# Kernel tuning notes

Hardware: AMD Instinct MI355X
Metric: run time of the kernel (lower is better)

Reference implementation:

```python
import jax, jax.numpy as jnp
import numpy as np

N_NODES = 65536
N_EDGES = 524288
N_GRAPHS = 512
G_NODES = 10000
NUM_DISEASES = 2000
IN_DIM = 128
HID = 256  # 2 * IN_DIM (z_emb concat feat)
D_FEAT = 512
C_FEAT = 512
MAX_Z = 4000


def setup_inputs() -> dict:
    key = jax.random.key(0)
    ks = jax.random.split(key, 20)
    rn = lambda k, shape: jax.random.normal(k, shape, dtype=jnp.float32) * 0.05
    return {
        "z": jax.random.randint(ks[0], (N_NODES,), 0, MAX_Z),
        "node_id": jnp.sort(jax.random.randint(ks[1], (N_NODES,), 0, G_NODES)),
        "src": jax.random.randint(ks[2], (N_EDGES,), 0, N_NODES),
        "dst": jax.random.randint(ks[3], (N_EDGES,), 0, N_NODES),
        "graph_ids": jnp.sort(jax.random.randint(ks[4], (N_NODES,), 0, N_GRAPHS)),
        "z_table": rn(ks[5], (MAX_Z, IN_DIM)),
        "d_feat_tab": rn(ks[6], (G_NODES, D_FEAT)),
        "c_feat_tab": rn(ks[7], (G_NODES, C_FEAT)),
        "Wd": rn(ks[8], (D_FEAT, IN_DIM)),
        "Wc": rn(ks[9], (C_FEAT, IN_DIM)),
        "gin_W1": rn(ks[10], (HID, HID)), "gin_b1": jnp.zeros((HID,), jnp.float32),
        "gin_W2": rn(ks[11], (HID, HID)), "gin_b2": jnp.zeros((HID,), jnp.float32),
        "sage_Wself": rn(ks[12], (HID, HID)),
        "sage_Wneigh": rn(ks[13], (HID, HID)),
        "sage_b": jnp.zeros((HID,), jnp.float32),
        "lin1_W": rn(ks[14], (HID, HID)), "lin1_b": jnp.zeros((HID,), jnp.float32),
        "lin2_W": rn(ks[15], (HID, 1)), "lin2_b": jnp.zeros((1,), jnp.float32),
    }


def reference(z, node_id, src, dst, graph_ids, z_table, d_feat_tab, c_feat_tab,
              Wd, Wc, gin_W1, gin_b1, gin_W2, gin_b2,
              sage_Wself, sage_Wneigh, sage_b, lin1_W, lin1_b, lin2_W, lin2_b):
    # --- input feature construction (Model.forward) ---
    z_emb = z_table[z]                               # [N, IN_DIM]
    d_proj = d_feat_tab[node_id] @ Wd                # d_fc (bias=False)
    c_proj = c_feat_tab[node_id] @ Wc                # c_fc (bias=False)
    disease = (node_id <= NUM_DISEASES)[:, None]
    # node_id is sorted -> masked concat order == node order
    feat = jnp.where(disease, d_proj, c_proj)        # [N, IN_DIM]
    x = jnp.concatenate([z_emb, feat], axis=1)       # [N, HID]
    # --- GINConv: sum aggregation, eps=0, mlp = Lin->ReLU->Lin ---
    agg = jax.ops.segment_sum(x[src], dst, num_segments=N_NODES)
    h = x + agg
    h = jax.nn.relu(h @ gin_W1 + gin_b1) @ gin_W2 + gin_b2
    # --- SAGEConv('mean'): fc_self(h) + fc_neigh(mean_neighbors) + bias ---
    deg = jax.ops.segment_sum(jnp.ones((N_EDGES,), h.dtype), dst, num_segments=N_NODES)
    mean_n = jax.ops.segment_sum(h[src], dst, num_segments=N_NODES) / jnp.maximum(deg, 1.0)[:, None]
    h = h @ sage_Wself + mean_n @ sage_Wneigh + sage_b
    # --- per-graph max pooling readout ---
    g = jax.ops.segment_max(h, graph_ids, num_segments=N_GRAPHS, indices_are_sorted=True)
    g = jnp.where(jnp.isfinite(g), g, 0.0)           # guard empty graphs
    # --- head: Linear -> ReLU -> (dropout p=0, eval) -> Linear ---
    h = jax.nn.relu(g @ lin1_W + lin1_b)
    return h @ lin2_W + lin2_b                       # [N_GRAPHS, 1]
```

## Files before the change

kernel.cpp:

```cpp
#include <hip/hip_runtime.h>
#include <hip/hip_bf16.h>

#define N_NODES     65536
#define N_EDGES     524288
#define N_GRAPHS    512
#define G_NODES_N   10000
#define NUM_DIS     2000
#define IN_DIM      128
#define HID         256
#define D_FEAT      512
#define MAX_Z       4000
#define POOL_SPLIT  8

typedef _Float16 half8 __attribute__((ext_vector_type(8)));
typedef float    f32x4 __attribute__((ext_vector_type(4)));

typedef __attribute__((address_space(1))) const void as1_void;
typedef __attribute__((address_space(3))) void       as3_void;

__global__ __launch_bounds__(256) void prep_kernel(
    const float* __restrict__ Ws, const float* __restrict__ Wn,
    const float* __restrict__ Wd, const float* __restrict__ Wc,
    const float* __restrict__ W1, const float* __restrict__ W2,
    const float* __restrict__ z_table,
    const int* __restrict__ z, const int* __restrict__ node_id,
    _Float16* __restrict__ WsT, _Float16* __restrict__ WnT,
    _Float16* __restrict__ WdT, _Float16* __restrict__ WcT,
    _Float16* __restrict__ W12P, _Float16* __restrict__ zt16,
    int2* __restrict__ zn2, int* __restrict__ cnt, int* __restrict__ flags)
{
    const int b = blockIdx.x;
    const int tid = threadIdx.x;
    if (b < 64) {
        __shared__ float tile[64][65];
        const float* W; _Float16* T; int K, N, k0, n0;
        if (b < 32) {
            const int mat = b >> 4, t = b & 15;
            K = HID; N = HID; k0 = (t >> 2) * 64; n0 = (t & 3) * 64;
            W = (mat == 0) ? Ws : Wn;
            T = (mat == 0) ? WsT : WnT;
        } else {
            const int bb = b - 32;
            const int mat = bb >> 4, t = bb & 15;
            K = D_FEAT; N = IN_DIM; k0 = (t >> 1) * 64; n0 = (t & 1) * 64;
            W = (mat == 0) ? Wd : Wc;
            T = (mat == 0) ? WdT : WcT;
        }
        const int tx = tid & 63, ty = tid >> 6;
        #pragma unroll
        for (int r = 0; r < 64; r += 4)
            tile[r + ty][tx] = W[(size_t)(k0 + r + ty) * N + n0 + tx];
        __syncthreads();
        #pragma unroll
        for (int c = 0; c < 64; c += 4)
            T[(size_t)(n0 + c + ty) * K + k0 + tx] = (_Float16)tile[tx][c + ty];
    } else if (b < 576) {
        const int bb = b - 64;
        const int mat = bb >> 8;
        const int k = bb & 255;
        const int n = tid;
        const float* W = mat ? W2 : W1;
        const float v = W[(size_t)k * HID + n];
        const size_t idx = (size_t)(mat * 8 + (k >> 5)) * 8192
                         + (size_t)((((k >> 3) & 3) * 256 + n) * 8 + (k & 7));
        W12P[idx] = (_Float16)v;
    } else if (b < 826) {
        const size_t base = ((size_t)(b - 576) * 256 + tid) * 8;
        const float4 f0 = *(const float4*)(z_table + base);
        const float4 f1 = *(const float4*)(z_table + base + 4);
        half8 h;
        h[0]=(_Float16)f0.x; h[1]=(_Float16)f0.y; h[2]=(_Float16)f0.z; h[3]=(_Float16)f0.w;
        h[4]=(_Float16)f1.x; h[5]=(_Float16)f1.y; h[6]=(_Float16)f1.z; h[7]=(_Float16)f1.w;
        *(half8*)(zt16 + base) = h;
    } else if (b < 890) {
        const int base = (b - 826) * 1024 + tid * 4;
        *(int4*)(cnt + base) = make_int4(0, 0, 0, 0);
        if (b == 826 && tid < 128) flags[tid] = 0;
    } else {
        const int i = (b - 890) * 256 + tid;
        zn2[i] = make_int2(z[i], node_id[i]);
    }
}

__global__ __launch_bounds__(256) void proj_mfma_kernel(
    const float* __restrict__ dtab, const float* __restrict__ ctab,
    const _Float16* __restrict__ WdT, const _Float16* __restrict__ WcT,
    _Float16* __restrict__ proj)
{
    __shared__ _Float16 Alds[128 * 40];
    __shared__ _Float16 Blds[128 * 40];
    const int blk = blockIdx.x;
    const float* tab; const _Float16* WT; int base, M, bm;
    if (blk < 16) { tab = dtab; WT = WdT; base = 0;           M = NUM_DIS + 1;             bm = blk * 128; }
    else          { tab = ctab; WT = WcT; base = NUM_DIS + 1; M = G_NODES_N - NUM_DIS - 1; bm = (blk - 16) * 128; }
    const int tid  = threadIdx.x;
    const int wave = tid >> 6, lane = tid & 63;
    const int q    = lane >> 4, l16 = lane & 15;
    const int mbase = (wave & 1) * 64, nbase = (wave >> 1) * 64;
    const int r = tid >> 1, s = tid & 1;

    f32x4 acc[4][4] = {};

    for (int kc = 0; kc < 16; ++kc) {
        const int k0 = kc * 32;
        const int arow = min(bm + r, M - 1);
        const float* gA = tab + (size_t)(base + arow) * D_FEAT + k0 + s * 16;
        const _Float16* gB = WT + (size_t)r * D_FEAT + k0 + s * 16;
        const float4 f0 = ((const float4*)gA)[0];
        const float4 f1 = ((const float4*)gA)[1];
        const float4 f2 = ((const float4*)gA)[2];
        const float4 f3 = ((const float4*)gA)[3];
        const half8 hb0 = *(const half8*)gB;
        const half8 hb1 = *(const half8*)(gB + 8);
        half8 h0, h1;
        h0[0]=(_Float16)f0.x; h0[1]=(_Float16)f0.y; h0[2]=(_Float16)f0.z; h0[3]=(_Float16)f0.w;
        h0[4]=(_Float16)f1.x; h0[5]=(_Float16)f1.y; h0[6]=(_Float16)f1.z; h0[7]=(_Float16)f1.w;
        h1[0]=(_Float16)f2.x; h1[1]=(_Float16)f2.y; h1[2]=(_Float16)f2.z; h1[3]=(_Float16)f2.w;
        h1[4]=(_Float16)f3.x; h1[5]=(_Float16)f3.y; h1[6]=(_Float16)f3.z; h1[7]=(_Float16)f3.w;
        __syncthreads();
        *(half8*)&Alds[r * 40 + s * 16]     = h0;
        *(half8*)&Alds[r * 40 + s * 16 + 8] = h1;
        *(half8*)&Blds[r * 40 + s * 16]     = hb0;
        *(half8*)&Blds[r * 40 + s * 16 + 8] = hb1;
        __syncthreads();
        half8 a[4], b[4];
        #pragma unroll
        for (int i = 0; i < 4; ++i)
            a[i] = *(const half8*)&Alds[(mbase + i * 16 + l16) * 40 + q * 8];
        #pragma unroll
        for (int j = 0; j < 4; ++j)
            b[j] = *(const half8*)&Blds[(nbase + j * 16 + l16) * 40 + q * 8];
        #pragma unroll
        for (int i = 0; i < 4; ++i)
            #pragma unroll
            for (int j = 0; j < 4; ++j)
                acc[i][j] = __builtin_amdgcn_mfma_f32_16x16x32_f16(a[i], b[j], acc[i][j], 0, 0, 0);
    }

    #pragma unroll
    for (int j = 0; j < 4; ++j) {
        const int colg = nbase + j * 16 + l16;
        #pragma unroll
        for (int i = 0; i < 4; ++i) {
            #pragma unroll
            for (int rr = 0; rr < 4; ++rr) {
                const int row = bm + mbase + i * 16 + q * 4 + rr;
                if (row < M)
                    proj[(size_t)(base + row) * IN_DIM + colg] = (_Float16)acc[i][j][rr];
            }
        }
    }
}

__global__ __launch_bounds__(256) void hist_kernel(
    const int* __restrict__ dst, int* __restrict__ cnt)
{
    const int e = blockIdx.x * 256 + threadIdx.x;
    if (e < N_EDGES) atomicAdd(&cnt[dst[e]], 1);
}

__global__ __launch_bounds__(256) void scan_fused_kernel(
    const int* __restrict__ cnt, int* __restrict__ row_ptr,
    int* __restrict__ fill, int* __restrict__ flags)
{
    __shared__ int a[256], b[256];
    __shared__ int sums[64];
    __shared__ int segbase;
    const int t = threadIdx.x;
    const int blk = blockIdx.x;
    const int base = blk * 1024 + t * 4;
    const int4 c = *(const int4*)(cnt + base);
    const int s = c.x + c.y + c.z + c.w;
    a[t] = s;
    __syncthreads();
    int* in = a; int* out = b;
    for (int off = 1; off < 256; off <<= 1) {
        out[t] = in[t] + ((t >= off) ? in[t - off] : 0);
        __syncthreads();
        int* tmp = in; in = out; out = tmp;
    }
    if (t == 0) {
        atomicExch(&flags[64 + blk], in[255]);
        __threadfence();
        atomicAdd(&flags[0], 1);
        while (atomicAdd(&flags[0], 0) < 64) {}
    }
    __syncthreads();
    if (t < 64) sums[t] = atomicAdd(&flags[64 + t], 0);
    __syncthreads();
    if (t == 0) {
        int pfx = 0;
        for (int i = 0; i < blk; ++i) pfx += sums[i];
        segbase = pfx;
        if (blk == 63) {
            int tot = pfx;
            for (int i = blk; i < 64; ++i) tot += sums[i];
            row_ptr[N_NODES] = tot;
        }
    }
    __syncthreads();
    const int run = in[t] - s + segbase;
    int4 r;
    r.x = run; r.y = run + c.x; r.z = r.y + c.y; r.w = r.z + c.z;
    *(int4*)(row_ptr + base) = r;
    *(int4*)(fill + base) = r;
}

__global__ __launch_bounds__(256) void scatter_kernel(
    const int* __restrict__ src, const int* __restrict__ dst,
    const int2* __restrict__ zn2,
    int* __restrict__ fill, int* __restrict__ col, int2* __restrict__ colzn)
{
    const int e = blockIdx.x * 256 + threadIdx.x;
    if (e < N_EDGES) {
        const int s = src[e];
        const int pos = atomicAdd(&fill[dst[e]], 1);
        col[pos] = s;
        colzn[pos] = zn2[s];
    }
}

__global__ __launch_bounds__(256) void gin_fused_kernel(
    const int* __restrict__ row_ptr, const int2* __restrict__ colzn,
    const int2* __restrict__ zn2,
    const _Float16* __restrict__ zt16, const _Float16* __restrict__ proj,
    const _Float16* __restrict__ W12P,
    const float* __restrict__ b1, const float* __restrict__ b2,
    _Float16* __restrict__ H)
{
    __shared__ _Float16 Apanel[32 * 264];
    __shared__ _Float16 Blds[2][8192];

    const int bm   = blockIdx.x * 32;
    const int tid  = threadIdx.x;
    const int wave = tid >> 6, lane = tid & 63;
    const int q    = lane >> 4, l16 = lane & 15;
    const int nbase = wave * 64;

    auto stage = [&](int c, int buf) {
        const _Float16* src = W12P + (size_t)c * 8192;
        #pragma unroll
        for (int tt = 0; tt < 4; ++tt) {
            const int seg = (wave * 4 + tt) * 64 + lane;
            __builtin_amdgcn_global_load_lds((as1_void*)(src + seg * 8),
                (as3_void*)&Blds[buf][(wave * 4 + tt) * 64 * 8], 16, 0, 0);
        }
    };

    stage(0, 0);

    {
        const int r = tid >> 3, p = tid & 7;
        const int gr = bm + r;
        const int beg = row_ptr[gr], end = row_ptr[gr + 1];
        float za[16], pa[16];
        {
            const int2 zn = zn2[gr];
            const half8* zp = (const half8*)(zt16 + (size_t)zn.x * IN_DIM + p * 16);
            const half8* pp = (const half8*)(proj + (size_t)zn.y * IN_DIM + p * 16);
            const half8 z0 = zp[0], z1 = zp[1], p0 = pp[0], p1 = pp[1];
            #pragma unroll
            for (int i = 0; i < 8; ++i) {
                za[i] = (float)z0[i]; za[8 + i] = (float)z1[i];
                pa[i] = (float)p0[i]; pa[8 + i] = (float)p1[i];
            }
        }
        int e = beg;
        for (; e + 2 <= end; e += 2) {
            const int2 znA = colzn[e];
            const int2 znB = colzn[e + 1];
            const half8* zpA = (const half8*)(zt16 + (size_t)znA.x * IN_DIM + p * 16);
            const half8* ppA = (const half8*)(proj + (size_t)znA.y * IN_DIM + p * 16);
            const half8* zpB = (const half8*)(zt16 + (size_t)znB.x * IN_DIM + p * 16);
            const half8* ppB = (const half8*)(proj + (size_t)znB.y * IN_DIM + p * 16);
            const half8 zA0 = zpA[0], zA1 = zpA[1], pA0 = ppA[0], pA1 = ppA[1];
            const half8 zB0 = zpB[0], zB1 = zpB[1], pB0 = ppB[0], pB1 = ppB[1];
            #pragma unroll
            for (int i = 0; i < 8; ++i) {
                za[i]     += (float)zA0[i] + (float)zB0[i];
                za[8 + i] += (float)zA1[i] + (float)zB1[i];
                pa[i]     += (float)pA0[i] + (float)pB0[i];
                pa[8 + i] += (float)pA1[i] + (float)pB1[i];
            }
        }
        if (e < end) {
            const int2 zn = colzn[e];
            const half8* zp = (const half8*)(zt16 + (size_t)zn.x * IN_DIM + p * 16);
            const half8* pp = (const half8*)(proj + (size_t)zn.y * IN_DIM + p * 16);
            const half8 z0 = zp[0], z1 = zp[1], p0 = pp[0], p1 = pp[1];
            #pragma unroll
            for (int i = 0; i < 8; ++i) {
                za[i] += (float)z0[i]; za[8 + i] += (float)z1[i];
                pa[i] += (float)p0[i]; pa[8 + i] += (float)p1[i];
            }
        }
        half8 oz0, oz1, op0, op1;
        #pragma unroll
        for (int i = 0; i < 8; ++i) {
            oz0[i] = (_Float16)za[i];     oz1[i] = (_Float16)za[8 + i];
            op0[i] = (_Float16)pa[i];     op1[i] = (_Float16)pa[8 + i];
        }
        *(half8*)&Apanel[r * 264 + p * 16]           = oz0;
        *(half8*)&Apanel[r * 264 + p * 16 + 8]       = oz1;
        *(half8*)&Apanel[r * 264 + 128 + p * 16]     = op0;
        *(half8*)&Apanel[r * 264 + 128 + p * 16 + 8] = op1;
    }
    __syncthreads();

    f32x4 acc[2][4] = {};
    int pb = 0;
    for (int c = 0; c < 16; ++c) {
        if (c + 1 < 16) stage(c + 1, pb ^ 1);
        if (c == 8) {
            #pragma unroll
            for (int j = 0; j < 4; ++j) {
                const int colg = nbase + j * 16 + l16;
                const float bv = b1[colg];
                #pragma unroll
                for (int i = 0; i < 2; ++i)
                    #pragma unroll
                    for (int rr = 0; rr < 4; ++rr) {
                        const float v = fmaxf(acc[i][j][rr] + bv, 0.0f);
                        Apanel[(i * 16 + q * 4 + rr) * 264 + colg] = (_Float16)v;
                        acc[i][j][rr] = 0.0f;
                    }
            }
            __syncthreads();
        }
        const int kl = (c & 7) * 32;
        half8 a[2], b[4];
        #pragma unroll
        for (int i = 0; i < 2; ++i)
            a[i] = *(const half8*)&Apanel[(i * 16 + l16) * 264 + kl + q * 8];
        #pragma unroll
        for (int j = 0; j < 4; ++j)
            b[j] = *(const half8*)&Blds[pb][(q * 256 + nbase + j * 16 + l16) * 8];
        #pragma unroll
        for (int i = 0; i < 2; ++i)
            #pragma unroll
            for (int j = 0; j < 4; ++j)
                acc[i][j] = __builtin_amdgcn_mfma_f32_16x16x32_f16(a[i], b[j], acc[i][j], 0, 0, 0);
        __syncthreads();
        pb ^= 1;
    }

    #pragma unroll
    for (int j = 0; j < 4; ++j) {
        const int colg = nbase + j * 16 + l16;
        const float bv = b2[colg];
        #pragma unroll
        for (int i = 0; i < 2; ++i)
            #pragma unroll
            for (int rr = 0; rr < 4; ++rr) {
                const int rowg = bm + i * 16 + q * 4 + rr;
                H[(size_t)rowg * HID + colg] = (_Float16)(acc[i][j][rr] + bv);
            }
    }
}

__global__ __launch_bounds__(256) void csr_agg_kernel(
    const int* __restrict__ row_ptr, const int* __restrict__ col,
    const _Float16* __restrict__ F, _Float16* __restrict__ OUT)
{
    const int t = blockIdx.x * 256 + threadIdx.x;
    const int d = t >> 5;
    const int q = t & 31;
    const int beg = row_ptr[d];
    const int end = row_ptr[d + 1];
    float acc[8] = {0.f,0.f,0.f,0.f,0.f,0.f,0.f,0.f};
    int e = beg;
    for (; e + 4 <= end; e += 4) {
        const int s0 = col[e],     s1 = col[e + 1];
        const int s2 = col[e + 2], s3 = col[e + 3];
        const half8 v0 = *(const half8*)(F + (size_t)s0 * HID + q * 8);
        const half8 v1 = *(const half8*)(F + (size_t)s1 * HID + q * 8);
        const half8 v2 = *(const half8*)(F + (size_t)s2 * HID + q * 8);
        const half8 v3 = *(const half8*)(F + (size_t)s3 * HID + q * 8);
        #pragma unroll
        for (int i = 0; i < 8; ++i)
            acc[i] += ((float)v0[i] + (float)v1[i]) + ((float)v2[i] + (float)v3[i]);
    }
    for (; e < end; ++e) {
        const half8 v0 = *(const half8*)(F + (size_t)col[e] * HID + q * 8);
        #pragma unroll
        for (int i = 0; i < 8; ++i) acc[i] += (float)v0[i];
    }
    const float rs = 1.0f / fmaxf((float)(end - beg), 1.0f);
    half8 o;
    #pragma unroll
    for (int i = 0; i < 8; ++i) o[i] = (_Float16)(acc[i] * rs);
    *(half8*)(OUT + (size_t)d * HID + q * 8) = o;
}

__global__ __launch_bounds__(256) void mfma_gemm_kernel(
    const _Float16* __restrict__ A1, const _Float16* __restrict__ A2,
    const _Float16* __restrict__ B1T, const _Float16* __restrict__ B2T,
    const float* __restrict__ bias, _Float16* __restrict__ Ch)
{
    __shared__ _Float16 Alds[128 * 32];
    __shared__ _Float16 Blds[128 * 32];
    const int bm   = blockIdx.x * 128;
    const int bn   = blockIdx.y * 128;
    const int tid  = threadIdx.x;
    const int wave = tid >> 6, lane = tid & 63;
    const int q    = lane >> 4, l16 = lane & 15;
    const int mbase = (wave & 1) * 64, nbase = (wave >> 1) * 64;

    f32x4 acc[4][4] = {};

    for (int kc = 0; kc < 16; ++kc) {
        const int k0 = (kc & 7) * 32;
        const _Float16* Abase = (kc < 8) ? A1 : A2;
        const _Float16* Bbase = (kc < 8) ? B1T : B2T;
        __syncthreads();
        #pragma unroll
        for (int t = 0; t < 2; ++t) {
            const int i   = wave * 128 + t * 64 + lane;
            const int row = i >> 2, s = i & 3;
            const _Float16* gA = Abase + (size_t)(bm + row) * HID + k0 + s * 8;
            const _Float16* gB = Bbase + (size_t)(bn + row) * HID + k0 + s * 8;
            __builtin_amdgcn_global_load_lds(
                (as1_void*)gA, (as3_void*)&Alds[(wave * 128 + t * 64) * 8], 16, 0, 0);
            __builtin_amdgcn_global_load_lds(
                (as1_void*)gB, (as3_void*)&Blds[(wave * 128 + t * 64) * 8], 16, 0, 0);
        }
        __syncthreads();
        half8 a[4], b[4];
        #pragma unroll
        for (int i = 0; i < 4; ++i)
            a[i] = *(const half8*)&Alds[(mbase + i * 16 + l16) * 32 + q * 8];
        #pragma unroll
        for (int j = 0; j < 4; ++j)
            b[j] = *(const half8*)&Blds[(nbase + j * 16 + l16) * 32 + q * 8];
        #pragma unroll
        for (int i = 0; i < 4; ++i)
            #pragma unroll
            for (int j = 0; j < 4; ++j)
                acc[i][j] = __builtin_amdgcn_mfma_f32_16x16x32_f16(a[i], b[j], acc[i][j], 0, 0, 0);
    }

    #pragma unroll
    for (int j = 0; j < 4; ++j) {
        const int colg = bn + nbase + j * 16 + l16;
        const float bv = bias[colg];
        #pragma unroll
        for (int i = 0; i < 4; ++i) {
            #pragma unroll
            for (int rr = 0; rr < 4; ++rr) {
                const int rowg = bm + mbase + i * 16 + q * 4 + rr;
                Ch[(size_t)rowg * HID + colg] = (_Float16)(acc[i][j][rr] + bv);
            }
        }
    }
}

__global__ __launch_bounds__(256) void pool_part_kernel(
    const _Float16* __restrict__ H2, const int* __restrict__ gid,
    float* __restrict__ Gpart)
{
    const int g = blockIdx.y;
    const int sp = blockIdx.x;
    const int j = threadIdx.x;
    int lo = 0, hi = N_NODES;
    while (lo < hi) { const int mid = (lo + hi) >> 1; if (gid[mid] < g) lo = mid + 1; else hi = mid; }
    const int start = lo;
    hi = N_NODES;
    while (lo < hi) { const int mid = (lo + hi) >> 1; if (gid[mid] < g + 1) lo = mid + 1; else hi = mid; }
    const int end = lo;
    float m = -INFINITY;
    for (int i = start + sp; i < end; i += POOL_SPLIT)
        m = fmaxf(m, (float)H2[(size_t)i * HID + j]);
    Gpart[((size_t)g * POOL_SPLIT + sp) * HID + j] = m;
}

__global__ __launch_bounds__(256) void head_kernel(
    const float* __restrict__ Gpart,
    const float* __restrict__ W1, const float* __restrict__ b1,
    const float* __restrict__ W2, const float* __restrict__ b2,
    float* __restrict__ out)
{
    const int g = blockIdx.x;
    const int j = threadIdx.x;
    __shared__ float row[HID];
    __shared__ float red[HID];
    float m = -INFINITY;
    #pragma unroll
    for (int sp = 0; sp < POOL_SPLIT; ++sp)
        m = fmaxf(m, Gpart[((size_t)g * POOL_SPLIT + sp) * HID + j]);
    row[j] = (m == -INFINITY) ? 0.0f : m;
    __syncthreads();
    float acc = b1[j];
    #pragma unroll 8
    for (int k = 0; k < HID; ++k)
        acc = fmaf(row[k], W1[k * HID + j], acc);
    acc = fmaxf(acc, 0.f);
    red[j] = acc * W2[j];
    __syncthreads();
    for (int s = 128; s > 0; s >>= 1) {
        if (j < s) red[j] += red[j + s];
        __syncthreads();
    }
    if (j == 0) out[g] = red[0] + b2[0];
}

extern "C" void kernel_launch(void* const* d_in, const int* in_sizes, int n_in,
                              void* d_out, int out_size, void* d_ws, size_t ws_size,
                              hipStream_t stream)
{
    const int*   z         = (const int*)d_in[0];
    const int*   node_id   = (const int*)d_in[1];
    const int*   src       = (const int*)d_in[2];
    const int*   dst       = (const int*)d_in[3];
    const int*   graph_ids = (const int*)d_in[4];
    const float* z_table   = (const float*)d_in[5];
    const float* d_feat    = (const float*)d_in[6];
    const float* c_feat    = (const float*)d_in[7];
    const float* Wd        = (const float*)d_in[8];
    const float* Wc        = (const float*)d_in[9];
    const float* gin_W1    = (const float*)d_in[10];
    const float* gin_b1    = (const float*)d_in[11];
    const float* gin_W2    = (const float*)d_in[12];
    const float* gin_b2    = (const float*)d_in[13];
    const float* sage_Wself  = (const float*)d_in[14];
    const float* sage_Wneigh = (const float*)d_in[15];
    const float* sage_b    = (const float*)d_in[16];
    const float* lin1_W    = (const float*)d_in[17];
    const float* lin1_b    = (const float*)d_in[18];
    const float* lin2_W    = (const float*)d_in[19];
    const float* lin2_b    = (const float*)d_in[20];
    float* out = (float*)d_out;

    const size_t NH = (size_t)N_NODES * HID;
    char* wsb = (char*)d_ws;
    _Float16* Hh   = (_Float16*)wsb;                     wsb += NH * 2;
    _Float16* AGGh = (_Float16*)wsb;                     wsb += NH * 2;
    _Float16* H2h  = (_Float16*)wsb;                     wsb += NH * 2;
    _Float16* projh= (_Float16*)wsb;                     wsb += (size_t)G_NODES_N * IN_DIM * 2;
    _Float16* W12P = (_Float16*)wsb;                     wsb += 16 * 8192 * 2;
    _Float16* WsT  = (_Float16*)wsb;                     wsb += HID * HID * 2;
    _Float16* WnT  = (_Float16*)wsb;                     wsb += HID * HID * 2;
    _Float16* WdT  = (_Float16*)wsb;                     wsb += D_FEAT * IN_DIM * 2;
    _Float16* WcT  = (_Float16*)wsb;                     wsb += D_FEAT * IN_DIM * 2;
    _Float16* zt16 = (_Float16*)wsb;                     wsb += (size_t)MAX_Z * IN_DIM * 2;
    int2* zn2      = (int2*)wsb;                         wsb += (size_t)N_NODES * 8;
    int2* colzn    = (int2*)wsb;                         wsb += (size_t)N_EDGES * 8;
    float* Gpart   = (float*)wsb;                        wsb += (size_t)N_GRAPHS * POOL_SPLIT * HID * 4;
    int* row_ptr   = (int*)wsb;                          wsb += (N_NODES + 4) * 4;
    int* cnt       = (int*)wsb;                          wsb += N_NODES * 4;
    int* fill      = (int*)wsb;                          wsb += N_NODES * 4;
    int* col       = (int*)wsb;                          wsb += N_EDGES * 4;
    int* flags     = (int*)wsb;                          wsb += 128 * 4;

    prep_kernel<<<1146, 256, 0, stream>>>(
        sage_Wself, sage_Wneigh, Wd, Wc, gin_W1, gin_W2, z_table, z, node_id,
        WsT, WnT, WdT, WcT, W12P, zt16, zn2, cnt, flags);

    hist_kernel<<<N_EDGES / 256, 256, 0, stream>>>(dst, cnt);
    scan_fused_kernel<<<64, 256, 0, stream>>>(cnt, row_ptr, fill, flags);
    scatter_kernel<<<N_EDGES / 256, 256, 0, stream>>>(src, dst, zn2, fill, col, colzn);

    proj_mfma_kernel<<<16 + 63, 256, 0, stream>>>(d_feat, c_feat, WdT, WcT, projh);

    gin_fused_kernel<<<N_NODES / 32, 256, 0, stream>>>(
        row_ptr, colzn, zn2, zt16, projh, W12P, gin_b1, gin_b2, Hh);

    csr_agg_kernel<<<(N_NODES * 32) / 256, 256, 0, stream>>>(row_ptr, col, Hh, AGGh);

    dim3 ggrid(N_NODES / 128, HID / 128);
    mfma_gemm_kernel<<<ggrid, 256, 0, stream>>>(Hh, AGGh, WsT, WnT, sage_b, H2h);

    dim3 pgrid(POOL_SPLIT, N_GRAPHS);
    pool_part_kernel<<<pgrid, 256, 0, stream>>>(H2h, graph_ids, Gpart);
    head_kernel<<<N_GRAPHS, 256, 0, stream>>>(Gpart, lin1_W, lin1_b, lin2_W, lin2_b, out);
}
```

Measured before the change: 366.9 us.

## Prefetch next K tile in projection and GEMM kernels; unroll edge gather by four

The projection GEMM now issues the global loads for the next K chunk into registers right after the LDS barrier, so the loads overlap the MFMA work. The main MFMA GEMM gets double-buffered LDS, with global_load_lds for the next stage issued before computing the current one, which drops one barrier per iteration. The GIN gather loop is unrolled from two to four edges to keep more loads in flight. These add register and LDS pressure, which may lower occupancy.

```diff
diff --git a/kernel.cpp b/kernel.cpp
--- a/kernel.cpp
+++ b/kernel.cpp
@@ -98,31 +98,38 @@
     const int q    = lane >> 4, l16 = lane & 15;
     const int mbase = (wave & 1) * 64, nbase = (wave >> 1) * 64;
     const int r = tid >> 1, s = tid & 1;
-
-    f32x4 acc[4][4] = {};
-
-    for (int kc = 0; kc < 16; ++kc) {
+    const int arow = min(bm + r, M - 1);
+
+    float4 fA[4]; half8 hB[2];
+    auto gload = [&](int kc) {
         const int k0 = kc * 32;
-        const int arow = min(bm + r, M - 1);
         const float* gA = tab + (size_t)(base + arow) * D_FEAT + k0 + s * 16;
         const _Float16* gB = WT + (size_t)r * D_FEAT + k0 + s * 16;
-        const float4 f0 = ((const float4*)gA)[0];
-        const float4 f1 = ((const float4*)gA)[1];
-        const float4 f2 = ((const float4*)gA)[2];
-        const float4 f3 = ((const float4*)gA)[3];
-        const half8 hb0 = *(const half8*)gB;
-        const half8 hb1 = *(const half8*)(gB + 8);
+        fA[0] = ((const float4*)gA)[0];
+        fA[1] = ((const float4*)gA)[1];
+        fA[2] = ((const float4*)gA)[2];
+        fA[3] = ((const float4*)gA)[3];
+        hB[0] = *(const half8*)gB;
+        hB[1] = *(const half8*)(gB + 8);
+    };
+
+    f32x4 acc[4][4] = {};
+    gload(0);
+
+    for (int kc = 0; kc < 16; ++kc) {
         half8 h0, h1;
-        h0[0]=(_Float16)f0.x; h0[1]=(_Float16)f0.y; h0[2]=(_Float16)f0.z; h0[3]=(_Float16)f0.w;
-        h0[4]=(_Float16)f1.x; h0[5]=(_Float16)f1.y; h0[6]=(_Float16)f1.z; h0[7]=(_Float16)f1.w;
-        h1[0]=(_Float16)f2.x; h1[1]=(_Float16)f2.y; h1[2]=(_Float16)f2.z; h1[3]=(_Float16)f2.w;
-        h1[4]=(_Float16)f3.x; h1[5]=(_Float16)f3.y; h1[6]=(_Float16)f3.z; h1[7]=(_Float16)f3.w;
+        h0[0]=(_Float16)fA[0].x; h0[1]=(_Float16)fA[0].y; h0[2]=(_Float16)fA[0].z; h0[3]=(_Float16)fA[0].w;
+        h0[4]=(_Float16)fA[1].x; h0[5]=(_Float16)fA[1].y; h0[6]=(_Float16)fA[1].z; h0[7]=(_Float16)fA[1].w;
+        h1[0]=(_Float16)fA[2].x; h1[1]=(_Float16)fA[2].y; h1[2]=(_Float16)fA[2].z; h1[3]=(_Float16)fA[2].w;
+        h1[4]=(_Float16)fA[3].x; h1[5]=(_Float16)fA[3].y; h1[6]=(_Float16)fA[3].z; h1[7]=(_Float16)fA[3].w;
+        const half8 wb0 = hB[0], wb1 = hB[1];
         __syncthreads();
         *(half8*)&Alds[r * 40 + s * 16]     = h0;
         *(half8*)&Alds[r * 40 + s * 16 + 8] = h1;
-        *(half8*)&Blds[r * 40 + s * 16]     = hb0;
-        *(half8*)&Blds[r * 40 + s * 16 + 8] = hb1;
-        __syncthreads();
+        *(half8*)&Blds[r * 40 + s * 16]     = wb0;
+        *(half8*)&Blds[r * 40 + s * 16 + 8] = wb1;
+        __syncthreads();
+        if (kc + 1 < 16) gload(kc + 1);
         half8 a[4], b[4];
         #pragma unroll
         for (int i = 0; i < 4; ++i)
@@ -266,24 +273,32 @@
             }
         }
         int e = beg;
-        for (; e + 2 <= end; e += 2) {
-            const int2 znA = colzn[e];
-            const int2 znB = colzn[e + 1];
-            const half8* zpA = (const half8*)(zt16 + (size_t)znA.x * IN_DIM + p * 16);
-            const half8* ppA = (const half8*)(proj + (size_t)znA.y * IN_DIM + p * 16);
-            const half8* zpB = (const half8*)(zt16 + (size_t)znB.x * IN_DIM + p * 16);
-            const half8* ppB = (const half8*)(proj + (size_t)znB.y * IN_DIM + p * 16);
-            const half8 zA0 = zpA[0], zA1 = zpA[1], pA0 = ppA[0], pA1 = ppA[1];
-            const half8 zB0 = zpB[0], zB1 = zpB[1], pB0 = ppB[0], pB1 = ppB[1];
+        for (; e + 4 <= end; e += 4) {
+            const int2 cA = colzn[e];
+            const int2 cB = colzn[e + 1];
+            const int2 cC = colzn[e + 2];
+            const int2 cD = colzn[e + 3];
+            const half8* zpA = (const half8*)(zt16 + (size_t)cA.x * IN_DIM + p * 16);
+            const half8* ppA = (const half8*)(proj + (size_t)cA.y * IN_DIM + p * 16);
+            const half8* zpB = (const half8*)(zt16 + (size_t)cB.x * IN_DIM + p * 16);
+            const half8* ppB = (const half8*)(proj + (size_t)cB.y * IN_DIM + p * 16);
+            const half8* zpC = (const half8*)(zt16 + (size_t)cC.x * IN_DIM + p * 16);
+            const half8* ppC = (const half8*)(proj + (size_t)cC.y * IN_DIM + p * 16);
+            const half8* zpD = (const half8*)(zt16 + (size_t)cD.x * IN_DIM + p * 16);
+            const half8* ppD = (const half8*)(proj + (size_t)cD.y * IN_DIM + p * 16);
+            const half8 zA0 = zpA[0], zA1 = zpA[1], qA0 = ppA[0], qA1 = ppA[1];
+            const half8 zB0 = zpB[0], zB1 = zpB[1], qB0 = ppB[0], qB1 = ppB[1];
+            const half8 zC0 = zpC[0], zC1 = zpC[1], qC0 = ppC[0], qC1 = ppC[1];
+            const half8 zD0 = zpD[0], zD1 = zpD[1], qD0 = ppD[0], qD1 = ppD[1];
             #pragma unroll
             for (int i = 0; i < 8; ++i) {
-                za[i]     += (float)zA0[i] + (float)zB0[i];
-                za[8 + i] += (float)zA1[i] + (float)zB1[i];
-                pa[i]     += (float)pA0[i] + (float)pB0[i];
-                pa[8 + i] += (float)pA1[i] + (float)pB1[i];
-            }
-        }
-        if (e < end) {
+                za[i]     += ((float)zA0[i] + (float)zB0[i]) + ((float)zC0[i] + (float)zD0[i]);
+                za[8 + i] += ((float)zA1[i] + (float)zB1[i]) + ((float)zC1[i] + (float)zD1[i]);
+                pa[i]     += ((float)qA0[i] + (float)qB0[i]) + ((float)qC0[i] + (float)qD0[i]);
+                pa[8 + i] += ((float)qA1[i] + (float)qB1[i]) + ((float)qC1[i] + (float)qD1[i]);
+            }
+        }
+        for (; e < end; ++e) {
             const int2 zn = colzn[e];
             const half8* zp = (const half8*)(zt16 + (size_t)zn.x * IN_DIM + p * 16);
             const half8* pp = (const half8*)(proj + (size_t)zn.y * IN_DIM + p * 16);
@@ -397,8 +412,8 @@
     const _Float16* __restrict__ B1T, const _Float16* __restrict__ B2T,
     const float* __restrict__ bias, _Float16* __restrict__ Ch)
 {
-    __shared__ _Float16 Alds[128 * 32];
-    __shared__ _Float16 Blds[128 * 32];
+    __shared__ _Float16 Alds[2][128 * 32];
+    __shared__ _Float16 Blds[2][128 * 32];
     const int bm   = blockIdx.x * 128;
     const int bn   = blockIdx.y * 128;
     const int tid  = threadIdx.x;
@@ -406,37 +421,44 @@
     const int q    = lane >> 4, l16 = lane & 15;
     const int mbase = (wave & 1) * 64, nbase = (wave >> 1) * 64;
 
-    f32x4 acc[4][4] = {};
-
-    for (int kc = 0; kc < 16; ++kc) {
+    auto stage = [&](int kc, int buf) {
         const int k0 = (kc & 7) * 32;
         const _Float16* Abase = (kc < 8) ? A1 : A2;
         const _Float16* Bbase = (kc < 8) ? B1T : B2T;
-        __syncthreads();
         #pragma unroll
         for (int t = 0; t < 2; ++t) {
             const int i   = wave * 128 + t * 64 + lane;
             const int row = i >> 2, s = i & 3;
-            const _Float16* gA = Abase + (size_t)(bm + row) * HID + k0 + s * 8;
-            const _Float16* gB = Bbase + (size_t)(bn + row) * HID + k0 + s * 8;
             __builtin_amdgcn_global_load_lds(
-                (as1_void*)gA, (as3_void*)&Alds[(wave * 128 + t * 64) * 8], 16, 0, 0);
+                (as1_void*)(Abase + (size_t)(bm + row) * HID + k0 + s * 8),
+                (as3_void*)&Alds[buf][(wave * 128 + t * 64) * 8], 16, 0, 0);
             __builtin_amdgcn_global_load_lds(
-                (as1_void*)gB, (as3_void*)&Blds[(wave * 128 + t * 64) * 8], 16, 0, 0);
-        }
-        __syncthreads();
+                (as1_void*)(Bbase + (size_t)(bn + row) * HID + k0 + s * 8),
+                (as3_void*)&Blds[buf][(wave * 128 + t * 64) * 8], 16, 0, 0);
+        }
+    };
+
+    f32x4 acc[4][4] = {};
+    stage(0, 0);
+    __syncthreads();
+
+    int pb = 0;
+    for (int kc = 0; kc < 16; ++kc) {
+        if (kc + 1 < 16) stage(kc + 1, pb ^ 1);
         half8 a[4], b[4];
         #pragma unroll
         for (int i = 0; i < 4; ++i)
-            a[i] = *(const half8*)&Alds[(mbase + i * 16 + l16) * 32 + q * 8];
+            a[i] = *(const half8*)&Alds[pb][(mbase + i * 16 + l16) * 32 + q * 8];
         #pragma unroll
         for (int j = 0; j < 4; ++j)
-            b[j] = *(const half8*)&Blds[(nbase + j * 16 + l16) * 32 + q * 8];
+            b[j] = *(const half8*)&Blds[pb][(nbase + j * 16 + l16) * 32 + q * 8];
         #pragma unroll
         for (int i = 0; i < 4; ++i)
             #pragma unroll
             for (int j = 0; j < 4; ++j)
                 acc[i][j] = __builtin_amdgcn_mfma_f32_16x16x32_f16(a[i], b[j], acc[i][j], 0, 0, 0);
+        __syncthreads();
+        pb ^= 1;
     }
 
     #pragma unroll
```

Result: no change. 367.7 us (+0.2%).
